# Kernel optimization log

Hardware: AMD Instinct MI355X
Metric: run time of the kernel (lower is better)

The kernel has to match this reference:

```python
import jax, jax.numpy as jnp
import numpy as np

N = 50000          # nodes
E = 800000         # edges (avg degree 16)
T = 4              # edge types (edge_attr_dim)
H = 8              # heads
C1 = 16            # state_dim (per-head channels, layer 1)
C2 = 8             # out_dim  (per-head channels, layer 2)
D = 128            # node_attr_dim
NEG = -1e9         # masked-attention logit
LRELU_SLOPE = 0.2  # PyG GATConv default negative_slope


def setup_inputs() -> dict:
    key = jax.random.key(0)
    ks = jax.random.split(key, 12)
    x = jax.random.normal(ks[0], (N, D), jnp.float32)
    edge_src = jax.random.randint(ks[1], (E,), 0, N, jnp.int32)
    edge_dst = jax.random.randint(ks[2], (E,), 0, N, jnp.int32)
    edge_type = jax.random.randint(ks[3], (E,), 0, T, jnp.int32)
    W1 = jax.random.normal(ks[4], (T, D, H * C1), jnp.float32) * (1.0 / np.sqrt(D))
    a1_src = jax.random.normal(ks[5], (T, H, C1), jnp.float32) * 0.1
    a1_dst = jax.random.normal(ks[6], (T, H, C1), jnp.float32) * 0.1
    b1 = jnp.zeros((T, H * C1), jnp.float32)
    W2 = jax.random.normal(ks[7], (T, H * C1, H * C2), jnp.float32) * (1.0 / np.sqrt(H * C1))
    a2_src = jax.random.normal(ks[8], (T, H, C2), jnp.float32) * 0.1
    a2_dst = jax.random.normal(ks[9], (T, H, C2), jnp.float32) * 0.1
    b2 = jnp.zeros((T, H * C2), jnp.float32)
    return dict(x=x, edge_src=edge_src, edge_dst=edge_dst, edge_type=edge_type,
                W1=W1, a1_src=a1_src, a1_dst=a1_dst, b1=b1,
                W2=W2, a2_src=a2_src, a2_dst=a2_dst, b2=b2)


def gat_conv(x_in, W, a_src, a_dst, b, src, dst, mask, n):
    """One PyG-style GATConv (concat heads, eval mode) on masked edge list."""
    heads, c = a_src.shape
    h = (x_in @ W).reshape(n, heads, c)                       # [N,H,C]
    s_src = jnp.sum(h * a_src, axis=-1)                        # [N,H]
    s_dst = jnp.sum(h * a_dst, axis=-1)                        # [N,H]
    e = jax.nn.leaky_relu(s_src[src] + s_dst[dst], LRELU_SLOPE)  # [Et,H]
    e = jnp.where(mask[:, None], e, NEG)
    m = jax.ops.segment_max(e, dst, num_segments=n)            # [N,H]
    p = jnp.exp(e - m[dst]) * mask[:, None].astype(e.dtype)    # unnorm softmax
    denom = jax.ops.segment_sum(p, dst, num_segments=n)        # [N,H]
    msg = p[:, :, None] * h[src]                               # [Et,H,C]
    agg = jax.ops.segment_sum(msg, dst, num_segments=n)        # [N,H,C]
    out = agg / denom[:, :, None]
    return out.reshape(n, heads * c) + b


def reference(x, edge_src, edge_dst, edge_type, W1, a1_src, a1_dst, b1,
              W2, a2_src, a2_dst, b2):
    n = x.shape[0]
    loops = jnp.arange(n, dtype=edge_src.dtype)
    src = jnp.concatenate([edge_src, loops])   # self-loops appended (PyG default)
    dst = jnp.concatenate([edge_dst, loops])
    ones = jnp.ones((n,), bool)
    outs = []
    for t in range(T):
        mask = jnp.concatenate([edge_type == t, ones])
        h1 = gat_conv(x, W1[t], a1_src[t], a1_dst[t], b1[t], src, dst, mask, n)
        h1 = jax.nn.relu(h1)
        h2 = gat_conv(h1, W2[t], a2_src[t], a2_dst[t], b2[t], src, dst, mask, n)
        outs.append(h2)
    return jnp.concatenate(outs, axis=1)       # [N, T*H*C2]
```

## Files before the change

### kernel.cpp

```cpp
#include <hip/hip_runtime.h>
#include <cstddef>

constexpr int NN  = 50000;
constexpr int NE  = 800000;
constexpr int NT  = 4;
constexpr int NH  = 8;
constexpr int C1  = 16;
constexpr int C2  = 8;
constexpr int DD  = 128;
constexpr int HC1 = NH * C1;
constexpr int HC2 = NH * C2;
constexpr int CAP = 22;
constexpr int BSTRIDE = 48;
constexpr float SLOPE = 0.2f;

constexpr int G_ZERO  = 2344;
constexpr int G_CONVB = 3125;
constexpr int G_P1    = NT * 16384 / 256;
constexpr int G_P2    = NT * 8192 / 256;
constexpr int G_SCATF = 782;
constexpr int G_GEMM  = (NN + 63) / 64;
constexpr int G_GAT1  = NN / 16;
constexpr int G_GAT2  = (NN + 31) / 32;

using short8 = __attribute__((ext_vector_type(8))) short;
using f32x4  = __attribute__((ext_vector_type(4))) float;
typedef unsigned short u16;

__device__ __forceinline__ float lrelu(float x) { return x > 0.f ? x : SLOPE * x; }
__device__ __forceinline__ float bfl(unsigned u) { return __uint_as_float(u << 16); }
__device__ __forceinline__ float bfh(unsigned u) { return __uint_as_float(u & 0xffff0000u); }
__device__ __forceinline__ u16 f2bf(float f) {
    unsigned u = __float_as_uint(f);
    return (u16)((u + 0x7fffu + ((u >> 16) & 1u)) >> 16);
}
__device__ __forceinline__ float dot8(uint4 hv, const float* a) {
    return bfl(hv.x) * a[0] + bfh(hv.x) * a[1] + bfl(hv.y) * a[2] + bfh(hv.y) * a[3]
         + bfl(hv.z) * a[4] + bfh(hv.z) * a[5] + bfl(hv.w) * a[6] + bfh(hv.w) * a[7];
}

__device__ __forceinline__ void scatter4(int e0, const int* __restrict__ esrc,
        const int* __restrict__ edst, const int* __restrict__ etyp,
        unsigned* __restrict__ bkt) {
    int bk[4], src[4];
    bool v[4];
    #pragma unroll
    for (int k = 0; k < 4; ++k) {
        int i = e0 + k * 256;
        v[k] = i < NE;
        bk[k] = 0; src[k] = 0;
        if (v[k]) { bk[k] = etyp[i] * NN + edst[i]; src[k] = esrc[i]; }
    }
    int slot[4];
    #pragma unroll
    for (int k = 0; k < 4; ++k)
        if (v[k]) slot[k] = atomicAdd((int*)((char*)bkt + (size_t)bk[k] * BSTRIDE), 1);
    #pragma unroll
    for (int k = 0; k < 4; ++k)
        if (v[k] && slot[k] < CAP)
            ((u16*)((char*)bkt + (size_t)bk[k] * BSTRIDE))[2 + slot[k]] = (u16)src[k];
}

template<bool XB>
__global__ __launch_bounds__(256) void init_kernel(const float* __restrict__ x,
        u16* __restrict__ xb, const float* __restrict__ W1, u16* __restrict__ wp1,
        const float* __restrict__ W2, u16* __restrict__ wp2,
        unsigned* __restrict__ bkt) {
    const int b = blockIdx.x, tid = threadIdx.x;
    const int CB = XB ? G_CONVB : 0;
    if (b < G_ZERO) {
        int i = b * 256 + tid;
        if (i < 600000) reinterpret_cast<uint4*>(bkt)[i] = make_uint4(0, 0, 0, 0);
    } else if (XB && b < G_ZERO + CB) {
        int i = (b - G_ZERO) * 256 + tid;
        float4 f0 = reinterpret_cast<const float4*>(x)[2 * i];
        float4 f1 = reinterpret_cast<const float4*>(x)[2 * i + 1];
        uint4 o;
        o.x = (unsigned)f2bf(f0.x) | ((unsigned)f2bf(f0.y) << 16);
        o.y = (unsigned)f2bf(f0.z) | ((unsigned)f2bf(f0.w) << 16);
        o.z = (unsigned)f2bf(f1.x) | ((unsigned)f2bf(f1.y) << 16);
        o.w = (unsigned)f2bf(f1.z) | ((unsigned)f2bf(f1.w) << 16);
        reinterpret_cast<uint4*>(xb)[i] = o;
    } else if (b < G_ZERO + CB + G_P1) {
        int i = (b - G_ZERO - CB) * 256 + tid;
        int t = i >> 14, r = i & 16383;
        int ntl = r >> 11, ks = (r >> 9) & 3, lane = (r >> 3) & 63, j = r & 7;
        int col = ntl * 16 + (lane & 15);
        int k   = ks * 32 + (lane >> 4) * 8 + j;
        wp1[i] = f2bf(W1[((size_t)t * DD + k) * HC1 + col]);
    } else {
        int i = (b - G_ZERO - CB - G_P1) * 256 + tid;
        int t = i >> 13, r = i & 8191;
        int ntl = r >> 11, ks = (r >> 9) & 3, lane = (r >> 3) & 63, j = r & 7;
        int col = ntl * 16 + (lane & 15);
        int k   = ks * 32 + (lane >> 4) * 8 + j;
        wp2[i] = f2bf(W2[((size_t)t * HC1 + k) * HC2 + col]);
    }
}

template<bool XB>
__device__ __forceinline__ void gemm1_body(int bx, int tid, const float* __restrict__ x,
        const u16* __restrict__ xb, const u16* __restrict__ Wp, u16* __restrict__ h1w) {
    constexpr int NTILE = HC1 / 16;
    const int wave = tid >> 6;
    const int lane = tid & 63;
    const int q    = lane >> 4;
    const int c    = lane & 15;
    const int rowbase = bx * 64 + wave * 16;

    int arow = rowbase + c; if (arow >= NN) arow = NN - 1;
    short8 afrag[4];
    if (XB) {
        const u16* ap = xb + (size_t)arow * DD + q * 8;
        #pragma unroll
        for (int ks = 0; ks < 4; ++ks)
            afrag[ks] = *reinterpret_cast<const short8*>(ap + ks * 32);
    } else {
        const float* xp = x + (size_t)arow * DD + q * 8;
        #pragma unroll
        for (int ks = 0; ks < 4; ++ks) {
            float4 f0 = *reinterpret_cast<const float4*>(xp + ks * 32);
            float4 f1 = *reinterpret_cast<const float4*>(xp + ks * 32 + 4);
            short8 a;
            a[0] = (short)f2bf(f0.x); a[1] = (short)f2bf(f0.y);
            a[2] = (short)f2bf(f0.z); a[3] = (short)f2bf(f0.w);
            a[4] = (short)f2bf(f1.x); a[5] = (short)f2bf(f1.y);
            a[6] = (short)f2bf(f1.z); a[7] = (short)f2bf(f1.w);
            afrag[ks] = a;
        }
    }

    f32x4 acc[NTILE];
    #pragma unroll
    for (int ntl = 0; ntl < NTILE; ++ntl) acc[ntl] = (f32x4){0.f, 0.f, 0.f, 0.f};
    const short8* wp = reinterpret_cast<const short8*>(Wp) + lane;
    #pragma unroll
    for (int ntl = 0; ntl < NTILE; ++ntl)
        #pragma unroll
        for (int ks = 0; ks < 4; ++ks) {
            short8 b = wp[(ntl * 4 + ks) * 64];
            acc[ntl] = __builtin_amdgcn_mfma_f32_16x16x32_bf16(afrag[ks], b, acc[ntl], 0, 0, 0);
        }

    #pragma unroll
    for (int ntl = 0; ntl < NTILE; ++ntl)
        #pragma unroll
        for (int reg = 0; reg < 4; ++reg) {
            int row = rowbase + q * 4 + reg;
            if (row < NN) h1w[(size_t)row * HC1 + ntl * 16 + c] = f2bf(acc[ntl][reg]);
        }
}

template<bool XB>
__global__ __launch_bounds__(256) void scatgemm_kernel(
        const int* __restrict__ esrc, const int* __restrict__ edst,
        const int* __restrict__ etyp, unsigned* __restrict__ bkt,
        const float* __restrict__ x, const u16* __restrict__ xb,
        const u16* __restrict__ wp1t, u16* __restrict__ h1) {
    const int b = blockIdx.x, tid = threadIdx.x;
    if (b < G_SCATF) scatter4(b * 1024 + tid, esrc, edst, etyp, bkt);
    else gemm1_body<XB>(b - G_SCATF, tid, x, xb, wp1t, h1);
}

template<int TPN, bool SPLIT>
__device__ __forceinline__ void gather_body(const unsigned* __restrict__ bkt, int bk,
        int q, const float* asr, float sdn, const uint4* __restrict__ h4,
        float& den, float acc[8]) {
    const uint2* bp = reinterpret_cast<const uint2*>((const char*)bkt + (size_t)bk * BSTRIDE);
    unsigned w[12];
    #pragma unroll
    for (int i = 0; i < 6; ++i) { uint2 u = bp[i]; w[2 * i] = u.x; w[2 * i + 1] = u.y; }
    int deg = (int)w[0]; if (deg > CAP) deg = CAP;
    #pragma unroll
    for (int c = 0; c < 6; ++c) {
        if (c * 4 >= deg) break;
        unsigned lo = w[1 + 2 * c];
        unsigned hi = (c < 5) ? w[2 + 2 * c] : 0u;
        int sv[4] = {(int)(lo & 0xffff), (int)(lo >> 16),
                     (int)(hi & 0xffff), (int)(hi >> 16)};
        #pragma unroll
        for (int j = 0; j < 4; ++j) {
            if (c * 4 + j < deg) {
                int sn = sv[j];
                uint4 hv = h4[(size_t)sn * TPN + q];
                float d = dot8(hv, asr);
                if (SPLIT) d += __shfl_xor(d, 1);
                float pp = __expf(lrelu(d + sdn));
                den += pp;
                acc[0] += pp * bfl(hv.x); acc[1] += pp * bfh(hv.x);
                acc[2] += pp * bfl(hv.y); acc[3] += pp * bfh(hv.y);
                acc[4] += pp * bfl(hv.z); acc[5] += pp * bfh(hv.z);
                acc[6] += pp * bfl(hv.w); acc[7] += pp * bfh(hv.w);
            }
        }
    }
}

__device__ __forceinline__ void g1g2_body(int bx, int tid, const unsigned* __restrict__ bkt,
        int t, const u16* __restrict__ h1r, const float* __restrict__ a1s_t,
        const float* __restrict__ a1d_t, const float* __restrict__ b1t,
        const u16* __restrict__ wp2t, u16* __restrict__ h2w) {
    __shared__ u16 lt[16][136];
    const int node0 = bx * 16;
    const int nl    = tid >> 4;
    const int node  = node0 + nl;
    const int q     = tid & 15;
    const int head  = q >> 1;
    const int bk    = t * NN + node;
    const uint4* __restrict__ h4 = reinterpret_cast<const uint4*>(h1r);

    float asr[8], adr[8];
    #pragma unroll
    for (int i = 0; i < 8; ++i) {
        asr[i] = a1s_t[head * C1 + (q & 1) * 8 + i];
        adr[i] = a1d_t[head * C1 + (q & 1) * 8 + i];
    }

    uint4 hv = h4[(size_t)node * 16 + q];
    float ds = dot8(hv, asr); ds += __shfl_xor(ds, 1);
    float dd = dot8(hv, adr); dd += __shfl_xor(dd, 1);
    const float sdn = dd;

    float p = __expf(lrelu(ds + sdn));
    float den = p;
    float acc[8];
    acc[0] = p * bfl(hv.x); acc[1] = p * bfh(hv.x);
    acc[2] = p * bfl(hv.y); acc[3] = p * bfh(hv.y);
    acc[4] = p * bfl(hv.z); acc[5] = p * bfh(hv.z);
    acc[6] = p * bfl(hv.w); acc[7] = p * bfh(hv.w);
    gather_body<16, true>(bkt, bk, q, asr, sdn, h4, den, acc);

    float inv = 1.f / den;
    uint4 ov;
    {
        float o[8];
        #pragma unroll
        for (int i = 0; i < 8; ++i)
            o[i] = fmaxf(acc[i] * inv + b1t[q * 8 + i], 0.f);
        ov.x = (unsigned)f2bf(o[0]) | ((unsigned)f2bf(o[1]) << 16);
        ov.y = (unsigned)f2bf(o[2]) | ((unsigned)f2bf(o[3]) << 16);
        ov.z = (unsigned)f2bf(o[4]) | ((unsigned)f2bf(o[5]) << 16);
        ov.w = (unsigned)f2bf(o[6]) | ((unsigned)f2bf(o[7]) << 16);
    }
    *reinterpret_cast<uint4*>(&lt[nl][q * 8]) = ov;
    __syncthreads();

    const int wave = tid >> 6;
    const int lane = tid & 63;
    const int quad = lane >> 4;
    const int c    = lane & 15;
    short8 af[4];
    #pragma unroll
    for (int ks = 0; ks < 4; ++ks)
        af[ks] = *reinterpret_cast<const short8*>(&lt[c][ks * 32 + quad * 8]);
    f32x4 cacc = (f32x4){0.f, 0.f, 0.f, 0.f};
    const short8* wp = reinterpret_cast<const short8*>(wp2t) + lane;
    #pragma unroll
    for (int ks = 0; ks < 4; ++ks)
        cacc = __builtin_amdgcn_mfma_f32_16x16x32_bf16(af[ks], wp[(wave * 4 + ks) * 64], cacc, 0, 0, 0);

    const int col = wave * 16 + c;
    #pragma unroll
    for (int reg = 0; reg < 4; ++reg) {
        int row = node0 + quad * 4 + reg;
        h2w[(size_t)row * HC2 + col] = f2bf(cacc[reg]);
    }
}

__device__ __forceinline__ void gat2_body(int bx, int tid, const unsigned* __restrict__ bkt,
        int t, const u16* __restrict__ h2r, const float* __restrict__ a2s_t,
        const float* __restrict__ a2d_t, const float* __restrict__ b2t,
        float* __restrict__ out) {
    const int node = bx * 32 + (tid >> 3);
    if (node >= NN) return;
    const int q    = tid & 7;
    const int head = q;
    const int bk   = t * NN + node;
    const uint4* __restrict__ h4 = reinterpret_cast<const uint4*>(h2r);

    float asr[8], adr[8];
    #pragma unroll
    for (int i = 0; i < 8; ++i) {
        asr[i] = a2s_t[head * C2 + i];
        adr[i] = a2d_t[head * C2 + i];
    }

    uint4 hv = h4[(size_t)node * 8 + q];
    const float sdn = dot8(hv, adr);
    float p = __expf(lrelu(dot8(hv, asr) + sdn));
    float den = p;
    float acc[8];
    acc[0] = p * bfl(hv.x); acc[1] = p * bfh(hv.x);
    acc[2] = p * bfl(hv.y); acc[3] = p * bfh(hv.y);
    acc[4] = p * bfl(hv.z); acc[5] = p * bfh(hv.z);
    acc[6] = p * bfl(hv.w); acc[7] = p * bfh(hv.w);
    gather_body<8, false>(bkt, bk, q, asr, sdn, h4, den, acc);

    float inv = 1.f / den;
    float o[8];
    #pragma unroll
    for (int i = 0; i < 8; ++i) o[i] = acc[i] * inv + b2t[q * 8 + i];
    float* op = out + (size_t)node * (NT * HC2) + t * HC2 + q * 8;
    reinterpret_cast<float4*>(op)[0] = make_float4(o[0], o[1], o[2], o[3]);
    reinterpret_cast<float4*>(op)[1] = make_float4(o[4], o[5], o[6], o[7]);
}

template<bool XB>
__global__ __launch_bounds__(256) void mega_kernel(
        int ngemm, int ng1, const unsigned* __restrict__ bkt,
        int t1, const u16* __restrict__ h1r, const float* __restrict__ a1s_t,
        const float* __restrict__ a1d_t, const float* __restrict__ b1t,
        const u16* __restrict__ wp2t, u16* __restrict__ h2w,
        int t2, const u16* __restrict__ h2r, const float* __restrict__ a2s_t,
        const float* __restrict__ a2d_t, const float* __restrict__ b2t,
        float* __restrict__ out,
        const float* __restrict__ x, const u16* __restrict__ xb,
        const u16* __restrict__ wp1n, u16* __restrict__ h1w) {
    const int b = blockIdx.x, tid = threadIdx.x;
    if (b < ngemm) {
        gemm1_body<XB>(b, tid, x, xb, wp1n, h1w);
    } else if (b < ngemm + ng1) {
        g1g2_body(b - ngemm, tid, bkt, t1, h1r, a1s_t, a1d_t, b1t, wp2t, h2w);
    } else {
        gat2_body(b - ngemm - ng1, tid, bkt, t2, h2r, a2s_t, a2d_t, b2t, out);
    }
}

template<bool XB>
static void run_pipeline(const float* x, const int* esrc, const int* edst,
        const int* etyp, const float* W1, const float* a1s, const float* a1d,
        const float* b1, const float* W2, const float* a2s, const float* a2d,
        const float* b2, float* out, char* base, hipStream_t stream) {
    size_t off = 0;
    u16* xb = nullptr;
    if (XB) { xb = (u16*)base; off += 12800000; }
    u16* h1d[2] = {(u16*)(base + off), (u16*)(base + off + 12800000)};
    off += 25600000;
    u16* h2d[2] = {(u16*)(base + off), (u16*)(base + off + 6400000)};
    off += 12800000;
    unsigned* bkt = (unsigned*)(base + off); off += 9600000;
    u16* wp1 = (u16*)(base + off); off += 131072;
    u16* wp2 = (u16*)(base + off);

    dim3 blk(256);
    int g_init = G_ZERO + (XB ? G_CONVB : 0) + G_P1 + G_P2;

    hipLaunchKernelGGL((init_kernel<XB>), dim3(g_init), blk, 0, stream,
                       x, xb, W1, wp1, W2, wp2, bkt);
    hipLaunchKernelGGL((scatgemm_kernel<XB>), dim3(G_SCATF + G_GEMM), blk, 0, stream,
                       esrc, edst, etyp, bkt, x, xb, wp1, h1d[0]);

    for (int t = 0; t < 5; ++t) {
        int ng1   = (t < 4) ? G_GAT1 : 0;
        int ngat2 = (t >= 1) ? G_GAT2 : 0;
        int ngemm = (t < 3) ? G_GEMM : 0;
        int grid  = ngemm + ng1 + ngat2;
        int tm = (t < 4) ? t : 3;
        int tp = (t < 3) ? t + 1 : 0;
        int t2 = (t >= 1) ? t - 1 : 0;
        hipLaunchKernelGGL((mega_kernel<XB>), dim3(grid), blk, 0, stream,
                           ngemm, ng1, bkt,
                           tm, h1d[tm & 1], a1s + tm * NH * C1, a1d + tm * NH * C1,
                           b1 + tm * HC1, wp2 + (size_t)tm * 8192, h2d[tm & 1],
                           t2, h2d[t2 & 1], a2s + t2 * NH * C2, a2d + t2 * NH * C2,
                           b2 + t2 * HC2, out,
                           x, xb, wp1 + (size_t)tp * 16384, h1d[tp & 1]);
    }
}

extern "C" void kernel_launch(void* const* d_in, const int* in_sizes, int n_in,
                              void* d_out, int out_size, void* d_ws, size_t ws_size,
                              hipStream_t stream) {
    const float* x    = (const float*)d_in[0];
    const int*   esrc = (const int*)d_in[1];
    const int*   edst = (const int*)d_in[2];
    const int*   etyp = (const int*)d_in[3];
    const float* W1   = (const float*)d_in[4];
    const float* a1s  = (const float*)d_in[5];
    const float* a1d  = (const float*)d_in[6];
    const float* b1   = (const float*)d_in[7];
    const float* W2   = (const float*)d_in[8];
    const float* a2s  = (const float*)d_in[9];
    const float* a2d  = (const float*)d_in[10];
    const float* b2   = (const float*)d_in[11];
    float* out = (float*)d_out;
    char* base = (char*)d_ws;

    if (ws_size >= 61000000)
        run_pipeline<true>(x, esrc, edst, etyp, W1, a1s, a1d, b1,
                           W2, a2s, a2d, b2, out, base, stream);
    else
        run_pipeline<false>(x, esrc, edst, etyp, W1, a1s, a1d, b1,
                            W2, a2s, a2d, b2, out, base, stream);
}
```

Baseline: 281.8 us.

## Split edge bucketing by type and overlap it with type-0 attention work

The edge scatter into per-type buckets is split. The pre-loop kernel now scatters only type-0 edges and computes the layer-1 GEMM for types 0 and 1. The first mega-kernel iteration then scatters types 1–3 alongside the type-0 GAT1 blocks. The aim is to shorten the serial prologue by overlapping most of the atomic-heavy bucketing with attention compute. In exchange, every scatter pass reads all edge types twice, and the t=0 GAT1 blocks now share the GPU with concurrent atomic scatter traffic.

```diff
diff --git a/kernel.cpp b/kernel.cpp
--- a/kernel.cpp
+++ b/kernel.cpp
@@ -41,15 +41,19 @@
 
 __device__ __forceinline__ void scatter4(int e0, const int* __restrict__ esrc,
         const int* __restrict__ edst, const int* __restrict__ etyp,
-        unsigned* __restrict__ bkt) {
+        unsigned* __restrict__ bkt, int tmin, int tmax) {
     int bk[4], src[4];
     bool v[4];
     #pragma unroll
     for (int k = 0; k < 4; ++k) {
         int i = e0 + k * 256;
-        v[k] = i < NE;
         bk[k] = 0; src[k] = 0;
-        if (v[k]) { bk[k] = etyp[i] * NN + edst[i]; src[k] = esrc[i]; }
+        v[k] = false;
+        if (i < NE) {
+            int ty = etyp[i];
+            v[k] = (ty >= tmin) && (ty <= tmax);
+            if (v[k]) { bk[k] = ty * NN + edst[i]; src[k] = esrc[i]; }
+        }
     }
     int slot[4];
     #pragma unroll
@@ -156,10 +160,12 @@
         const int* __restrict__ esrc, const int* __restrict__ edst,
         const int* __restrict__ etyp, unsigned* __restrict__ bkt,
         const float* __restrict__ x, const u16* __restrict__ xb,
-        const u16* __restrict__ wp1t, u16* __restrict__ h1) {
+        const u16* __restrict__ wp1a, u16* __restrict__ h1a,
+        const u16* __restrict__ wp1b, u16* __restrict__ h1b) {
     const int b = blockIdx.x, tid = threadIdx.x;
-    if (b < G_SCATF) scatter4(b * 1024 + tid, esrc, edst, etyp, bkt);
-    else gemm1_body<XB>(b - G_SCATF, tid, x, xb, wp1t, h1);
+    if (b < G_SCATF) scatter4(b * 1024 + tid, esrc, edst, etyp, bkt, 0, 0);
+    else if (b < G_SCATF + G_GEMM) gemm1_body<XB>(b - G_SCATF, tid, x, xb, wp1a, h1a);
+    else gemm1_body<XB>(b - G_SCATF - G_GEMM, tid, x, xb, wp1b, h1b);
 }
 
 template<int TPN, bool SPLIT>
@@ -307,7 +313,9 @@
 
 template<bool XB>
 __global__ __launch_bounds__(256) void mega_kernel(
-        int ngemm, int ng1, const unsigned* __restrict__ bkt,
+        int nscat, int ngemm, int ng1,
+        const int* __restrict__ esrc, const int* __restrict__ edst,
+        const int* __restrict__ etyp, unsigned* __restrict__ bkt,
         int t1, const u16* __restrict__ h1r, const float* __restrict__ a1s_t,
         const float* __restrict__ a1d_t, const float* __restrict__ b1t,
         const u16* __restrict__ wp2t, u16* __restrict__ h2w,
@@ -317,12 +325,14 @@
         const float* __restrict__ x, const u16* __restrict__ xb,
         const u16* __restrict__ wp1n, u16* __restrict__ h1w) {
     const int b = blockIdx.x, tid = threadIdx.x;
-    if (b < ngemm) {
-        gemm1_body<XB>(b, tid, x, xb, wp1n, h1w);
-    } else if (b < ngemm + ng1) {
-        g1g2_body(b - ngemm, tid, bkt, t1, h1r, a1s_t, a1d_t, b1t, wp2t, h2w);
+    if (b < nscat) {
+        scatter4(b * 1024 + tid, esrc, edst, etyp, bkt, 1, 3);
+    } else if (b < nscat + ngemm) {
+        gemm1_body<XB>(b - nscat, tid, x, xb, wp1n, h1w);
+    } else if (b < nscat + ngemm + ng1) {
+        g1g2_body(b - nscat - ngemm, tid, bkt, t1, h1r, a1s_t, a1d_t, b1t, wp2t, h2w);
     } else {
-        gat2_body(b - ngemm - ng1, tid, bkt, t2, h2r, a2s_t, a2d_t, b2t, out);
+        gat2_body(b - nscat - ngemm - ng1, tid, bkt, t2, h2r, a2s_t, a2d_t, b2t, out);
     }
 }
 
@@ -347,24 +357,26 @@
 
     hipLaunchKernelGGL((init_kernel<XB>), dim3(g_init), blk, 0, stream,
                        x, xb, W1, wp1, W2, wp2, bkt);
-    hipLaunchKernelGGL((scatgemm_kernel<XB>), dim3(G_SCATF + G_GEMM), blk, 0, stream,
-                       esrc, edst, etyp, bkt, x, xb, wp1, h1d[0]);
+    hipLaunchKernelGGL((scatgemm_kernel<XB>), dim3(G_SCATF + 2 * G_GEMM), blk, 0, stream,
+                       esrc, edst, etyp, bkt, x, xb,
+                       wp1, h1d[0], wp1 + 16384, h1d[1]);
 
     for (int t = 0; t < 5; ++t) {
+        int nscat = (t == 0) ? G_SCATF : 0;
+        int ngemm = (t == 1 || t == 2) ? G_GEMM : 0;
         int ng1   = (t < 4) ? G_GAT1 : 0;
         int ngat2 = (t >= 1) ? G_GAT2 : 0;
-        int ngemm = (t < 3) ? G_GEMM : 0;
-        int grid  = ngemm + ng1 + ngat2;
+        int grid  = nscat + ngemm + ng1 + ngat2;
         int tm = (t < 4) ? t : 3;
-        int tp = (t < 3) ? t + 1 : 0;
+        int tg = (t == 1 || t == 2) ? t + 1 : 0;
         int t2 = (t >= 1) ? t - 1 : 0;
         hipLaunchKernelGGL((mega_kernel<XB>), dim3(grid), blk, 0, stream,
-                           ngemm, ng1, bkt,
+                           nscat, ngemm, ng1, esrc, edst, etyp, bkt,
                            tm, h1d[tm & 1], a1s + tm * NH * C1, a1d + tm * NH * C1,
                            b1 + tm * HC1, wp2 + (size_t)tm * 8192, h2d[tm & 1],
                            t2, h2d[t2 & 1], a2s + t2 * NH * C2, a2d + t2 * NH * C2,
                            b2 + t2 * HC2, out,
-                           x, xb, wp1 + (size_t)tp * 16384, h1d[tp & 1]);
+                           x, xb, wp1 + (size_t)tg * 16384, h1d[tg & 1]);
     }
 }
 
```

Measured after the change: 284.3 us. About the same (+0.9%).
